# Kernel optimization log

Measured on AMD Instinct MI355X. Metric: run time of the kernel, lower is better.

## Reference

```python
import jax, jax.numpy as jnp
import numpy as np

NUM_ITERATIONS = 3


def _squash_elementwise(s):
    # Faithful to original: squared_norm summed over trailing axis of size 1
    # => elementwise squash v = s^2 * s / ((1 + s^2) * sqrt(s^2))
    sq = s * s
    return sq * s / ((1.0 + sq) * jnp.sqrt(sq))


def setup_inputs() -> dict:
    key = jax.random.key(0)
    k1, k2 = jax.random.split(key)
    B, R, C, O, I = 256, 1152, 10, 16, 8
    x = jax.random.normal(k1, (B, R, I), dtype=jnp.float32)
    W = jax.random.normal(k2, (R, C, O, I), dtype=jnp.float32)
    return {"x": x, "W": W}


def reference(x, W):
    # x: (B, R, I); W: (R, C, O, I)
    R, C, O, I = W.shape
    # u_hat[b,r,c,o] = sum_i W[r,c,o,i] * x[b,r,i]   (matmul W @ x per route/capsule)
    u_hat = jnp.einsum('rcoi,bri->brco', W, x)  # (B, R, C, O)
    b_ij = jnp.zeros((R, C), dtype=x.dtype)  # batch-shared routing logits
    v = None
    for it in range(NUM_ITERATIONS):
        c_ij = jax.nn.softmax(b_ij, axis=0)  # softmax over routes (dim=1 in torch)
        s_j = jnp.einsum('rc,brco->bco', c_ij, u_hat)  # weighted sum over routes
        v = _squash_elementwise(s_j)  # (B, C, O)
        if it < NUM_ITERATIONS - 1:
            # agreement a[b,r,c] = u_hat[b,r,c,:] . v[b,c,:]
            a_ij = jnp.einsum('brco,bco->brc', u_hat, v)
            b_ij = b_ij + a_ij.mean(axis=0)  # mean over batch, batch-shared update
    return v[..., None]  # (B, C, O, 1) matches v_j.squeeze(1)
```

## Files before the change

### kernel.cpp

```cpp
#include <hip/hip_runtime.h>

static constexpr int B_ = 256;
static constexpr int R_ = 1152;
static constexpr int C_ = 10;
static constexpr int O_ = 16;
static constexpr int I_ = 8;
static constexpr int SCO = C_ * O_;
static constexpr int K_ = R_ * I_;

typedef short bf16x8 __attribute__((ext_vector_type(8)));
typedef float f32x4  __attribute__((ext_vector_type(4)));

__device__ __forceinline__ unsigned short f2bf(float f) {
  union { float f; unsigned int u; } c; c.f = f;
  const unsigned int u = c.u;
  return (unsigned short)((u + 0x7fffu + ((u >> 16) & 1u)) >> 16);
}
__device__ __forceinline__ float bf2f(unsigned short h) {
  union { unsigned int u; float f; } c; c.u = ((unsigned int)h) << 16; return c.f;
}

__global__ __launch_bounds__(256) void prep0(const float* __restrict__ x,
                                             const float* __restrict__ W,
                                             unsigned short* __restrict__ xb,
                                             unsigned short* __restrict__ wb,
                                             unsigned short* __restrict__ wraw,
                                             unsigned short* __restrict__ xT) {
  const int bx = blockIdx.x;
  const int t  = threadIdx.x;
  if (bx < 256) {
    const float4* wf = (const float4*)W;
    ushort4* wo = (ushort4*)wb;
    ushort4* wr = (ushort4*)wraw;
    for (int idx = bx * 256 + t; idx < (R_ * C_ * O_ * I_) / 4; idx += 65536) {
      const float4 v4 = wf[idx];
      ushort4 s4, r4;
      s4.x = f2bf(v4.x * (1.0f / 1152.0f)); s4.y = f2bf(v4.y * (1.0f / 1152.0f));
      s4.z = f2bf(v4.z * (1.0f / 1152.0f)); s4.w = f2bf(v4.w * (1.0f / 1152.0f));
      r4.x = f2bf(v4.x); r4.y = f2bf(v4.y); r4.z = f2bf(v4.z); r4.w = f2bf(v4.w);
      wo[idx] = s4; wr[idx] = r4;
    }
  } else {
    __shared__ float sx[18 * 8 * 68];
    const int idx2 = bx - 256;
    const int bq = idx2 & 3, rseg = idx2 >> 2;
    const int rbase = rseg * 18;
    for (int idx = t; idx < 64 * 36; idx += 256) {
      const int b = idx / 36, f4 = idx - b * 36;
      const size_t off = (size_t)(bq * 64 + b) * K_ + rbase * I_ + f4 * 4;
      const float4 val = *(const float4*)(x + off);
      ushort4 o4;
      o4.x = f2bf(val.x); o4.y = f2bf(val.y); o4.z = f2bf(val.z); o4.w = f2bf(val.w);
      *(ushort4*)(xb + off) = o4;
      const int rr = f4 >> 1, i4 = (f4 & 1) * 4;
      sx[(rr * 8 + i4 + 0) * 68 + b] = val.x;
      sx[(rr * 8 + i4 + 1) * 68 + b] = val.y;
      sx[(rr * 8 + i4 + 2) * 68 + b] = val.z;
      sx[(rr * 8 + i4 + 3) * 68 + b] = val.w;
    }
    __syncthreads();
    const int lane = t & 63, w = t >> 6;
    for (int row = w * 36; row < w * 36 + 36; ++row)
      xT[(size_t)(rbase * 8 + row) * 256 + bq * 64 + lane] = f2bf(sx[row * 68 + lane]);
  }
}

__global__ __launch_bounds__(512) void k_gemm(const unsigned short* __restrict__ xb,
                                              const unsigned short* __restrict__ wb,
                                              unsigned short* __restrict__ vb,
                                              float* __restrict__ out, int final_) {
  __shared__ float sred[8][16 * 17];
  const int bx = blockIdx.x;
  const int g = (bx & 7) * 20 + (bx >> 3);
  const int c = g >> 4, mtile = g & 15;
  const int t = threadIdx.x, lane = t & 63;
  const int w = __builtin_amdgcn_readfirstlane(t >> 6);
  const int mrow = lane & 15, quad = lane >> 4;
  const int m0 = mtile * 16;

  const unsigned short* ap = xb + (size_t)(m0 + mrow) * K_ + w * 1152 + quad * 8;
  const unsigned short* bp = wb + ((size_t)(w * 144 + quad) * C_ + c) * 128 + mrow * 8;
  f32x4 acc = {0.0f, 0.0f, 0.0f, 0.0f};
#pragma unroll 6
  for (int kk = 0; kk < 36; ++kk) {
    const bf16x8 a = *(const bf16x8*)(ap + kk * 32);
    const bf16x8 b = *(const bf16x8*)(bp + (size_t)kk * 4 * C_ * 128);
    acc = __builtin_amdgcn_mfma_f32_16x16x32_bf16(a, b, acc, 0, 0, 0);
  }
#pragma unroll
  for (int rg = 0; rg < 4; ++rg)
    sred[w][mrow * 17 + quad * 4 + rg] = acc[rg];
  __syncthreads();
  if (t < 256) {
    int m, n;
    if (final_) { m = t >> 4; n = t & 15; } else { n = t >> 4; m = t & 15; }
    const int e = n * 17 + m;
    const float s = ((sred[0][e] + sred[1][e]) + (sred[2][e] + sred[3][e]))
                  + ((sred[4][e] + sred[5][e]) + (sred[6][e] + sred[7][e]));
    const float val = s * fabsf(s) / (1.0f + s * s);
    if (final_) out[(size_t)(m0 + m) * SCO + c * 16 + n] = val;
    else        vb[(size_t)(c * 16 + n) * 256 + m0 + m] = f2bf(val);
  }
}

__global__ __launch_bounds__(256) void k_pv(const unsigned short* __restrict__ xT,
                                            const unsigned short* __restrict__ vb,
                                            const float* __restrict__ W,
                                            float* __restrict__ bsum) {
  __shared__ float sp[10 * 8 * 128];
  const int bx = blockIdx.x;
  const int seg = (bx & 7) * 18 + (bx >> 3);
  const int r0 = seg * 8;
  const int t = threadIdx.x, lane = t & 63;
  const int w = __builtin_amdgcn_readfirstlane(t >> 6);
  const int mrow = lane & 15, quad = lane >> 4;

  const unsigned short* ap = xT + (size_t)(seg * 64 + w * 16 + mrow) * 256 + quad * 8;
  const unsigned short* bp = vb + (size_t)mrow * 256 + quad * 8;
  bf16x8 afr[8];
#pragma unroll
  for (int kk = 0; kk < 8; ++kk) afr[kk] = *(const bf16x8*)(ap + kk * 32);

  f32x4 acc[10];
#pragma unroll
  for (int c = 0; c < 10; ++c) acc[c] = (f32x4){0.0f, 0.0f, 0.0f, 0.0f};
#pragma unroll
  for (int c = 0; c < 10; ++c) {
#pragma unroll
    for (int kk = 0; kk < 8; ++kk) {
      const bf16x8 b = *(const bf16x8*)(bp + (size_t)(c * 16) * 256 + kk * 32);
      acc[c] = __builtin_amdgcn_mfma_f32_16x16x32_bf16(afr[kk], b, acc[c], 0, 0, 0);
    }
  }
#pragma unroll
  for (int c = 0; c < 10; ++c)
#pragma unroll
    for (int rg = 0; rg < 4; ++rg) {
      const int ml = w * 16 + quad * 4 + rg;
      sp[(c * 8 + (ml >> 3)) * 128 + mrow * 8 + (ml & 7)] = acc[c][rg];
    }
  __syncthreads();
  const int p8 = t >> 5, l32 = t & 31;
#pragma unroll
  for (int ch = 0; ch < 10; ++ch) {
    const int pair = ch * 8 + p8;
    const int rl = pair / 10, c = pair - rl * 10;
    const float4 pv = *(const float4*)&sp[(c * 8 + rl) * 128 + l32 * 4];
    const float4 wv = *(const float4*)(W + (size_t)(r0 + rl) * 1280 + c * 128 + l32 * 4);
    float prod = wv.x * pv.x + wv.y * pv.y + wv.z * pv.z + wv.w * pv.w;
    prod += __shfl_xor(prod, 1);  prod += __shfl_xor(prod, 2);
    prod += __shfl_xor(prod, 4);  prod += __shfl_xor(prod, 8);
    prod += __shfl_xor(prod, 16);
    if (l32 == 0) bsum[(size_t)(r0 + rl) * C_ + c] = prod;
  }
}

__global__ __launch_bounds__(256) void k_bc(const float* __restrict__ bsum,
                                            const float* __restrict__ bvec_in,
                                            float* __restrict__ bvec_out,
                                            const unsigned short* __restrict__ wraw,
                                            unsigned short* __restrict__ wb,
                                            int first) {
  __shared__ float cl[R_];
  __shared__ float smx[4];
  __shared__ float sms[4];
  const int bx = blockIdx.x;
  const int c  = bx >> 3, rt = bx & 7;
  const int t  = threadIdx.x;
  float bv[5], ef[5];
  float mx = -3.402823466e38f;
#pragma unroll
  for (int k = 0; k < 5; ++k) {
    int r = t + k * 256;
    if (r < R_) {
      float val = bsum[(size_t)r * C_ + c] * (1.0f / 256.0f);
      if (!first) val += bvec_in[r * C_ + c];
      if (rt == 0) bvec_out[r * C_ + c] = val;
      bv[k] = val;
      mx = fmaxf(mx, val);
    }
  }
  mx = fmaxf(mx, __shfl_xor(mx, 1));  mx = fmaxf(mx, __shfl_xor(mx, 2));
  mx = fmaxf(mx, __shfl_xor(mx, 4));  mx = fmaxf(mx, __shfl_xor(mx, 8));
  mx = fmaxf(mx, __shfl_xor(mx, 16)); mx = fmaxf(mx, __shfl_xor(mx, 32));
  if ((t & 63) == 0) smx[t >> 6] = mx;
  __syncthreads();
  const float MX = fmaxf(fmaxf(smx[0], smx[1]), fmaxf(smx[2], smx[3]));
  float se = 0.0f;
#pragma unroll
  for (int k = 0; k < 5; ++k) {
    int r = t + k * 256;
    if (r < R_) { ef[k] = expf(bv[k] - MX); se += ef[k]; }
  }
  se += __shfl_xor(se, 1);  se += __shfl_xor(se, 2);  se += __shfl_xor(se, 4);
  se += __shfl_xor(se, 8);  se += __shfl_xor(se, 16); se += __shfl_xor(se, 32);
  if ((t & 63) == 0) sms[t >> 6] = se;
  __syncthreads();
  const float inv = 1.0f / ((sms[0] + sms[1]) + (sms[2] + sms[3]));
#pragma unroll
  for (int k = 0; k < 5; ++k) {
    int r = t + k * 256;
    if (r < R_) cl[r] = ef[k] * inv;
  }
  __syncthreads();
  for (int idx = t; idx < 144 * 128; idx += 256) {
    const int r = rt * 144 + (idx >> 7), j = idx & 127;
    const size_t a = ((size_t)r * C_ + c) * 128 + j;
    wb[a] = f2bf(bf2f(wraw[a]) * cl[r]);
  }
}

extern "C" void kernel_launch(void* const* d_in, const int* in_sizes, int n_in,
                              void* d_out, int out_size, void* d_ws, size_t ws_size,
                              hipStream_t stream) {
  const float* x = (const float*)d_in[0];
  const float* W = (const float*)d_in[1];
  float* out = (float*)d_out;
  float* ws = (float*)d_ws;

  float* bvecA = ws;
  float* bvecB = bvecA + (R_ * C_);
  float* bsum  = bvecB + (R_ * C_);
  unsigned short* xb   = (unsigned short*)(bsum + R_ * C_);
  unsigned short* wb   = xb + (size_t)B_ * K_;
  unsigned short* wraw = wb + (size_t)R_ * C_ * O_ * I_;
  unsigned short* xT   = wraw + (size_t)R_ * C_ * O_ * I_;
  unsigned short* vb   = xT + (size_t)R_ * 8 * 256;

  prep0<<<512, 256, 0, stream>>>(x, W, xb, wb, wraw, xT);
  for (int it = 0; it < 3; ++it) {
    k_gemm<<<160, 512, 0, stream>>>(xb, wb, vb, out, it == 2 ? 1 : 0);
    if (it < 2) {
      k_pv<<<144, 256, 0, stream>>>(xT, vb, W, bsum);
      k_bc<<<80, 256, 0, stream>>>(bsum, bvecA, (it == 0) ? bvecA : bvecB,
                                   wraw, wb, it == 0 ? 1 : 0);
    }
  }
}
```

Before: 163.5 us.

## Fold softmax normalization into GEMM epilogue, fuse bc into pv, split-K gemm

Removes the separate softmax/weight-scaling kernel. k_pv now computes the logit update, exp(b) and unnormalized scaled bf16 weights directly, and atomically accumulates the per-capsule partition sums Z. k_gemm divides by Z in its epilogue, which avoids a global max/normalize pass. The gemm is split along K into two halves across 320 blocks, combined through float atomics and a last-arriving-block counter, and k_pv stages vb in swizzled LDS. The risks are expf overflow without max subtraction, and extra atomic and sync traffic.

```diff
diff --git a/kernel.cpp b/kernel.cpp
--- a/kernel.cpp
+++ b/kernel.cpp
@@ -23,22 +23,25 @@
 __global__ __launch_bounds__(256) void prep0(const float* __restrict__ x,
                                              const float* __restrict__ W,
                                              unsigned short* __restrict__ xb,
-                                             unsigned short* __restrict__ wb,
                                              unsigned short* __restrict__ wraw,
-                                             unsigned short* __restrict__ xT) {
+                                             unsigned short* __restrict__ xT,
+                                             float* __restrict__ sbuf,
+                                             unsigned int* __restrict__ cnt,
+                                             float* __restrict__ Z) {
   const int bx = blockIdx.x;
   const int t  = threadIdx.x;
+  const int zi = bx * 256 + t;
+  if (zi < 3 * 160 * 256) sbuf[zi] = 0.0f;
+  if (zi < 512) cnt[zi] = 0u;
+  if (zi < 32)  Z[zi] = (zi < 10) ? 1152.0f : 0.0f;
   if (bx < 256) {
     const float4* wf = (const float4*)W;
-    ushort4* wo = (ushort4*)wb;
     ushort4* wr = (ushort4*)wraw;
     for (int idx = bx * 256 + t; idx < (R_ * C_ * O_ * I_) / 4; idx += 65536) {
       const float4 v4 = wf[idx];
-      ushort4 s4, r4;
-      s4.x = f2bf(v4.x * (1.0f / 1152.0f)); s4.y = f2bf(v4.y * (1.0f / 1152.0f));
-      s4.z = f2bf(v4.z * (1.0f / 1152.0f)); s4.w = f2bf(v4.w * (1.0f / 1152.0f));
+      ushort4 r4;
       r4.x = f2bf(v4.x); r4.y = f2bf(v4.y); r4.z = f2bf(v4.z); r4.w = f2bf(v4.w);
-      wo[idx] = s4; wr[idx] = r4;
+      wr[idx] = r4;
     }
   } else {
     __shared__ float sx[18 * 8 * 68];
@@ -66,23 +69,32 @@
 }
 
 __global__ __launch_bounds__(512) void k_gemm(const unsigned short* __restrict__ xb,
-                                              const unsigned short* __restrict__ wb,
+                                              const unsigned short* __restrict__ Bm,
+                                              const float* __restrict__ Zit,
                                               unsigned short* __restrict__ vb,
-                                              float* __restrict__ out, int final_) {
+                                              float* __restrict__ out,
+                                              float* __restrict__ sbuf,
+                                              unsigned int* __restrict__ cnt,
+                                              int final_) {
   __shared__ float sred[8][16 * 17];
+  __shared__ int sflag;
   const int bx = blockIdx.x;
-  const int g = (bx & 7) * 20 + (bx >> 3);
-  const int c = g >> 4, mtile = g & 15;
+  const int g = (bx & 7) * 40 + (bx >> 3);
+  const int mtile = g / 20;
+  const int rem = g - mtile * 20;
+  const int c = rem >> 1, sub = rem & 1;
   const int t = threadIdx.x, lane = t & 63;
   const int w = __builtin_amdgcn_readfirstlane(t >> 6);
   const int mrow = lane & 15, quad = lane >> 4;
   const int m0 = mtile * 16;
-
-  const unsigned short* ap = xb + (size_t)(m0 + mrow) * K_ + w * 1152 + quad * 8;
-  const unsigned short* bp = wb + ((size_t)(w * 144 + quad) * C_ + c) * 128 + mrow * 8;
+  const int kb = sub * 4608 + w * 576;
+  const int rb = sub * 576 + w * 72;
+
+  const unsigned short* ap = xb + (size_t)(m0 + mrow) * K_ + kb + quad * 8;
+  const unsigned short* bp = Bm + ((size_t)(rb + quad) * C_ + c) * 128 + mrow * 8;
   f32x4 acc = {0.0f, 0.0f, 0.0f, 0.0f};
 #pragma unroll 6
-  for (int kk = 0; kk < 36; ++kk) {
+  for (int kk = 0; kk < 18; ++kk) {
     const bf16x8 a = *(const bf16x8*)(ap + kk * 32);
     const bf16x8 b = *(const bf16x8*)(bp + (size_t)kk * 4 * C_ * 128);
     acc = __builtin_amdgcn_mfma_f32_16x16x32_bf16(a, b, acc, 0, 0, 0);
@@ -91,23 +103,38 @@
   for (int rg = 0; rg < 4; ++rg)
     sred[w][mrow * 17 + quad * 4 + rg] = acc[rg];
   __syncthreads();
+  const int tile = mtile * 10 + c;
+  int m = 0, n = 0;
   if (t < 256) {
-    int m, n;
     if (final_) { m = t >> 4; n = t & 15; } else { n = t >> 4; m = t & 15; }
     const int e = n * 17 + m;
-    const float s = ((sred[0][e] + sred[1][e]) + (sred[2][e] + sred[3][e]))
-                  + ((sred[4][e] + sred[5][e]) + (sred[6][e] + sred[7][e]));
-    const float val = s * fabsf(s) / (1.0f + s * s);
-    if (final_) out[(size_t)(m0 + m) * SCO + c * 16 + n] = val;
-    else        vb[(size_t)(c * 16 + n) * 256 + m0 + m] = f2bf(val);
+    const float val = ((sred[0][e] + sred[1][e]) + (sred[2][e] + sred[3][e]))
+                    + ((sred[4][e] + sred[5][e]) + (sred[6][e] + sred[7][e]));
+    atomicAdd(&sbuf[(size_t)tile * 256 + t], val);
+  }
+  __syncthreads();
+  if (t == 0) sflag = (int)atomicAdd(&cnt[tile], 1u);
+  __syncthreads();
+  if (sflag == 0) return;
+  if (t < 256) {
+    const float tot = atomicAdd(&sbuf[(size_t)tile * 256 + t], 0.0f);
+    const float s = tot / Zit[c];
+    const float v = s * fabsf(s) / (1.0f + s * s);
+    if (final_) out[(size_t)(m0 + m) * SCO + c * 16 + n] = v;
+    else        vb[(size_t)(c * 16 + n) * 256 + m0 + m] = f2bf(v);
   }
 }
 
 __global__ __launch_bounds__(256) void k_pv(const unsigned short* __restrict__ xT,
                                             const unsigned short* __restrict__ vb,
                                             const float* __restrict__ W,
-                                            float* __restrict__ bsum) {
-  __shared__ float sp[10 * 8 * 128];
+                                            const unsigned short* __restrict__ wraw,
+                                            unsigned short* __restrict__ wb2,
+                                            float* __restrict__ bvec,
+                                            float* __restrict__ Zout,
+                                            int first) {
+  __shared__ __align__(16) unsigned short svb[40960];
+  __shared__ float sbs[80];
   const int bx = blockIdx.x;
   const int seg = (bx & 7) * 18 + (bx >> 3);
   const int r0 = seg * 8;
@@ -116,22 +143,40 @@
   const int mrow = lane & 15, quad = lane >> 4;
 
   const unsigned short* ap = xT + (size_t)(seg * 64 + w * 16 + mrow) * 256 + quad * 8;
-  const unsigned short* bp = vb + (size_t)mrow * 256 + quad * 8;
   bf16x8 afr[8];
 #pragma unroll
   for (int kk = 0; kk < 8; ++kk) afr[kk] = *(const bf16x8*)(ap + kk * 32);
 
+  {
+    const char* src = (const char*)vb;
+    char* dst = (char*)svb;
+#pragma unroll
+    for (int i = 0; i < 20; ++i) {
+      const int ci = i * 256 + t;
+      const int lin = ci * 16;
+      const int n = ci >> 5;
+      *(bf16x8*)(dst + (lin ^ ((n & 7) << 4))) = *(const bf16x8*)(src + lin);
+    }
+  }
+  __syncthreads();
+
   f32x4 acc[10];
 #pragma unroll
   for (int c = 0; c < 10; ++c) acc[c] = (f32x4){0.0f, 0.0f, 0.0f, 0.0f};
 #pragma unroll
   for (int c = 0; c < 10; ++c) {
+    const int n = c * 16 + mrow;
+    const int base = n * 512 + quad * 16;
 #pragma unroll
     for (int kk = 0; kk < 8; ++kk) {
-      const bf16x8 b = *(const bf16x8*)(bp + (size_t)(c * 16) * 256 + kk * 32);
+      const bf16x8 b = *(const bf16x8*)((const char*)svb +
+                        ((base + kk * 64) ^ ((n & 7) << 4)));
       acc[c] = __builtin_amdgcn_mfma_f32_16x16x32_bf16(afr[kk], b, acc[c], 0, 0, 0);
     }
   }
+  __syncthreads();
+
+  float* sp = (float*)svb;
 #pragma unroll
   for (int c = 0; c < 10; ++c)
 #pragma unroll
@@ -140,6 +185,7 @@
       sp[(c * 8 + (ml >> 3)) * 128 + mrow * 8 + (ml & 7)] = acc[c][rg];
     }
   __syncthreads();
+
   const int p8 = t >> 5, l32 = t & 31;
 #pragma unroll
   for (int ch = 0; ch < 10; ++ch) {
@@ -151,62 +197,39 @@
     prod += __shfl_xor(prod, 1);  prod += __shfl_xor(prod, 2);
     prod += __shfl_xor(prod, 4);  prod += __shfl_xor(prod, 8);
     prod += __shfl_xor(prod, 16);
-    if (l32 == 0) bsum[(size_t)(r0 + rl) * C_ + c] = prod;
-  }
-}
-
-__global__ __launch_bounds__(256) void k_bc(const float* __restrict__ bsum,
-                                            const float* __restrict__ bvec_in,
-                                            float* __restrict__ bvec_out,
-                                            const unsigned short* __restrict__ wraw,
-                                            unsigned short* __restrict__ wb,
-                                            int first) {
-  __shared__ float cl[R_];
-  __shared__ float smx[4];
-  __shared__ float sms[4];
-  const int bx = blockIdx.x;
-  const int c  = bx >> 3, rt = bx & 7;
-  const int t  = threadIdx.x;
-  float bv[5], ef[5];
-  float mx = -3.402823466e38f;
-#pragma unroll
-  for (int k = 0; k < 5; ++k) {
-    int r = t + k * 256;
-    if (r < R_) {
-      float val = bsum[(size_t)r * C_ + c] * (1.0f / 256.0f);
-      if (!first) val += bvec_in[r * C_ + c];
-      if (rt == 0) bvec_out[r * C_ + c] = val;
-      bv[k] = val;
-      mx = fmaxf(mx, val);
-    }
-  }
-  mx = fmaxf(mx, __shfl_xor(mx, 1));  mx = fmaxf(mx, __shfl_xor(mx, 2));
-  mx = fmaxf(mx, __shfl_xor(mx, 4));  mx = fmaxf(mx, __shfl_xor(mx, 8));
-  mx = fmaxf(mx, __shfl_xor(mx, 16)); mx = fmaxf(mx, __shfl_xor(mx, 32));
-  if ((t & 63) == 0) smx[t >> 6] = mx;
-  __syncthreads();
-  const float MX = fmaxf(fmaxf(smx[0], smx[1]), fmaxf(smx[2], smx[3]));
-  float se = 0.0f;
-#pragma unroll
-  for (int k = 0; k < 5; ++k) {
-    int r = t + k * 256;
-    if (r < R_) { ef[k] = expf(bv[k] - MX); se += ef[k]; }
-  }
-  se += __shfl_xor(se, 1);  se += __shfl_xor(se, 2);  se += __shfl_xor(se, 4);
-  se += __shfl_xor(se, 8);  se += __shfl_xor(se, 16); se += __shfl_xor(se, 32);
-  if ((t & 63) == 0) sms[t >> 6] = se;
-  __syncthreads();
-  const float inv = 1.0f / ((sms[0] + sms[1]) + (sms[2] + sms[3]));
-#pragma unroll
-  for (int k = 0; k < 5; ++k) {
-    int r = t + k * 256;
-    if (r < R_) cl[r] = ef[k] * inv;
-  }
-  __syncthreads();
-  for (int idx = t; idx < 144 * 128; idx += 256) {
-    const int r = rt * 144 + (idx >> 7), j = idx & 127;
-    const size_t a = ((size_t)r * C_ + c) * 128 + j;
-    wb[a] = f2bf(bf2f(wraw[a]) * cl[r]);
+    if (l32 == 0) sbs[rl * 10 + c] = prod;
+  }
+  __syncthreads();
+
+  if (t < 80) {
+    const int rl = t / 10, c = t - rl * 10;
+    const int r = r0 + rl;
+    float b = sbs[t] * (1.0f / 256.0f);
+    if (!first) b += bvec[r * C_ + c];
+    bvec[r * C_ + c] = b;
+    sbs[t] = expf(b);
+  }
+  __syncthreads();
+  if (t < 10) {
+    float z = 0.0f;
+#pragma unroll
+    for (int rl = 0; rl < 8; ++rl) z += sbs[rl * 10 + t];
+    atomicAdd(&Zout[t], z);
+  }
+
+#pragma unroll
+  for (int i = 0; i < 5; ++i) {
+    const int base = i * 2048 + t * 8;
+    const int rl = base / 1280, rem2 = base - rl * 1280;
+    const int c = rem2 >> 7;
+    const float e = sbs[rl * 10 + c];
+    const size_t off = ((size_t)(r0 + rl) * C_ + c) * 128 + (rem2 & 127);
+    const bf16x8 wv8 = *(const bf16x8*)(wraw + off);
+    bf16x8 o8;
+#pragma unroll
+    for (int j = 0; j < 8; ++j)
+      o8[j] = (short)f2bf(bf2f((unsigned short)wv8[j]) * e);
+    *(bf16x8*)(wb2 + off) = o8;
   }
 }
 
@@ -216,24 +239,21 @@
   const float* x = (const float*)d_in[0];
   const float* W = (const float*)d_in[1];
   float* out = (float*)d_out;
-  float* ws = (float*)d_ws;
-
-  float* bvecA = ws;
-  float* bvecB = bvecA + (R_ * C_);
-  float* bsum  = bvecB + (R_ * C_);
-  unsigned short* xb   = (unsigned short*)(bsum + R_ * C_);
-  unsigned short* wb   = xb + (size_t)B_ * K_;
-  unsigned short* wraw = wb + (size_t)R_ * C_ * O_ * I_;
+
+  float* bvec = (float*)d_ws;
+  float* Z    = bvec + R_ * C_;
+  float* sbuf = Z + 32;
+  unsigned int* cnt = (unsigned int*)(sbuf + 3 * 160 * 256);
+  unsigned short* xb   = (unsigned short*)(cnt + 512);
+  unsigned short* wraw = xb + (size_t)B_ * K_;
   unsigned short* xT   = wraw + (size_t)R_ * C_ * O_ * I_;
   unsigned short* vb   = xT + (size_t)R_ * 8 * 256;
-
-  prep0<<<512, 256, 0, stream>>>(x, W, xb, wb, wraw, xT);
-  for (int it = 0; it < 3; ++it) {
-    k_gemm<<<160, 512, 0, stream>>>(xb, wb, vb, out, it == 2 ? 1 : 0);
-    if (it < 2) {
-      k_pv<<<144, 256, 0, stream>>>(xT, vb, W, bsum);
-      k_bc<<<80, 256, 0, stream>>>(bsum, bvecA, (it == 0) ? bvecA : bvecB,
-                                   wraw, wb, it == 0 ? 1 : 0);
-    }
-  }
-}
+  unsigned short* wb2  = vb + (size_t)160 * 256;
+
+  prep0<<<512, 256, 0, stream>>>(x, W, xb, wraw, xT, sbuf, cnt, Z);
+  k_gemm<<<320, 512, 0, stream>>>(xb, wraw, Z + 0,  vb, out, sbuf + 0 * 40960, cnt + 0,   0);
+  k_pv  <<<144, 256, 0, stream>>>(xT, vb, W, wraw, wb2, bvec, Z + 10, 1);
+  k_gemm<<<320, 512, 0, stream>>>(xb, wb2,  Z + 10, vb, out, sbuf + 1 * 40960, cnt + 160, 0);
+  k_pv  <<<144, 256, 0, stream>>>(xT, vb, W, wraw, wb2, bvec, Z + 20, 0);
+  k_gemm<<<320, 512, 0, stream>>>(xb, wb2,  Z + 20, vb, out, sbuf + 2 * 40960, cnt + 320, 1);
+}
```

After: 131.1 us. -19.8%, faster.
